# Kernel optimization log

Measured on AMD Instinct MI355X. Metric: run time of the kernel, lower is better.

## Reference

```python
import jax, jax.numpy as jnp
import numpy as np

B, S, D, H = 1, 2048, 1024, 16
DH = D // H  # 64
HID = 4 * D
EPS = 1e-5
NEG = -1.0e9


def setup_inputs() -> dict:
    key = jax.random.key(0)
    ks = jax.random.split(key, 12)
    s = 0.02
    return {
        "y": jax.random.normal(ks[0], (B, S, D), jnp.float32),
        "encoder_output": jax.random.normal(ks[1], (B, S, D), jnp.float32),
        # per-head shared projection (query_fc used for q,k,v — faithful to source bug)
        "Wq_self": jax.random.normal(ks[2], (H, D, DH), jnp.float32) * s,
        "bq_self": jax.random.normal(ks[3], (H, DH), jnp.float32) * s,
        "Wq_cross": jax.random.normal(ks[4], (H, D, DH), jnp.float32) * s,
        "bq_cross": jax.random.normal(ks[5], (H, DH), jnp.float32) * s,
        "g1": jnp.ones((D,), jnp.float32), "beta1": jnp.zeros((D,), jnp.float32),
        "g2": jnp.ones((D,), jnp.float32), "beta2": jnp.zeros((D,), jnp.float32),
        "g3": jnp.ones((D,), jnp.float32), "beta3": jnp.zeros((D,), jnp.float32),
        "w1": jax.random.normal(ks[6], (D, HID), jnp.float32) * s,
        "b1": jax.random.normal(ks[7], (HID,), jnp.float32) * s,
        "w2": jax.random.normal(ks[8], (HID, D), jnp.float32) * s,
        "b2": jax.random.normal(ks[9], (D,), jnp.float32) * s,
    }


def _layernorm(x, g, b):
    mu = jnp.mean(x, axis=-1, keepdims=True)
    var = jnp.mean((x - mu) ** 2, axis=-1, keepdims=True)
    return (x - mu) * jax.lax.rsqrt(var + EPS) * g + b


def _mha(x_q, x_kv, W, bias, causal):
    # source bug: q, k, v all use query_fc projection
    q = jnp.einsum('bsd,hde->bhse', x_q, W) + bias[None, :, None, :]
    k = jnp.einsum('bsd,hde->bhse', x_kv, W) + bias[None, :, None, :]
    v = jnp.einsum('bsd,hde->bhse', x_kv, W) + bias[None, :, None, :]
    scores = jnp.einsum('bhse,bhte->bhst', q, k) / jnp.sqrt(jnp.float32(DH))
    if causal:
        sq, sk = scores.shape[-2], scores.shape[-1]
        mask = jnp.triu(jnp.ones((sq, sk), bool), k=1)
        scores = jnp.where(mask, NEG, scores)
    p = jax.nn.softmax(scores, axis=-1)
    out = jnp.einsum('bhst,bhte->bhse', p, v)  # [B,H,S,DH]
    b, h, s, e = out.shape
    return out.transpose(0, 2, 1, 3).reshape(b, s, h * e)


def reference(y, encoder_output, Wq_self, bq_self, Wq_cross, bq_cross,
              g1, beta1, g2, beta2, g3, beta3, w1, b1, w2, b2):
    sa = _mha(y, y, Wq_self, bq_self, causal=True)
    y1 = _layernorm(y + sa, g1, beta1)
    ca = _mha(y1, encoder_output, Wq_cross, bq_cross, causal=False)
    y2 = _layernorm(y1 + ca, g2, beta2)
    ff = jnp.maximum(y2 @ w1 + b1, 0.0) @ w2 + b2
    return _layernorm(y2 + ff, g3, beta3)
```

## Files before the change

### kernel.cpp

```cpp
#include <hip/hip_runtime.h>
#include <hip/hip_bf16.h>


#define S_LEN 2048
#define DMODEL 1024
#define NHEAD 16
#define DHEAD 64
#define HIDDEN 4096

using bf16 = __hip_bfloat16;
typedef __attribute__((ext_vector_type(8))) short bf16x8;
typedef __attribute__((ext_vector_type(4))) float floatx4;

__device__ __forceinline__ void async_ld16(const void* g, void* l) {
  __builtin_amdgcn_global_load_lds(
      (const __attribute__((address_space(1))) unsigned int*)g,
      (__attribute__((address_space(3))) unsigned int*)l, 16, 0, 0);
}

__device__ __forceinline__ unsigned short f2bf_bits(float f) {
  __hip_bfloat16 b = __float2bfloat16(f);
  return *(unsigned short*)&b;
}

template <bool HEADB>
__global__ __launch_bounds__(256) void transp_bf16_kernel(
    const float* __restrict__ src0, bf16* __restrict__ dst0,
    const float* __restrict__ src1, bf16* __restrict__ dst1, int K, int N) {
  const float* src = blockIdx.z ? src1 : src0;
  bf16* dst = blockIdx.z ? dst1 : dst0;
  __shared__ float tile[32][33];
  const int tx = threadIdx.x & 31, ty = threadIdx.x >> 5;
  const int k0 = blockIdx.y * 32, n0 = blockIdx.x * 32;
#pragma unroll
  for (int i = 0; i < 4; ++i) {
    const int k = k0 + ty + i * 8;
    const int n = n0 + tx;
    size_t idx;
    if (HEADB)
      idx = (size_t)(n >> 6) * ((size_t)K * 64) + (size_t)k * 64 + (n & 63);
    else
      idx = (size_t)k * N + n;
    tile[ty + i * 8][tx] = src[idx];
  }
  __syncthreads();
#pragma unroll
  for (int i = 0; i < 4; ++i) {
    const int n = n0 + ty + i * 8;
    const int k = k0 + tx;
    dst[(size_t)n * K + k] = __float2bfloat16(tile[tx][ty + i * 8]);
  }
}

__global__ __launch_bounds__(256) void conv_bf16_kernel(
    const float* __restrict__ src0, bf16* __restrict__ dst0,
    const float* __restrict__ src1, bf16* __restrict__ dst1, int n4) {
  const float* src = blockIdx.z ? src1 : src0;
  bf16* dst = blockIdx.z ? dst1 : dst0;
  const int i = blockIdx.x * 256 + threadIdx.x;
  if (i >= n4) return;
  float4 v = ((const float4*)src)[i];
  unsigned short r[4] = {f2bf_bits(v.x), f2bf_bits(v.y), f2bf_bits(v.z), f2bf_bits(v.w)};
  ((ushort2*)dst)[i * 2] = make_ushort2(r[0], r[1]);
  ((ushort2*)dst)[i * 2 + 1] = make_ushort2(r[2], r[3]);
}

template <int BM, int BN, bool RELU, bool DUALT, typename CT>
__global__ __launch_bounds__(256) void mfma_gemm_kernel(
    const bf16* __restrict__ A0, const bf16* __restrict__ Bt0,
    const float* __restrict__ bias0, CT* __restrict__ C0,
    bf16* __restrict__ Ct0,
    const bf16* __restrict__ A1, const bf16* __restrict__ Bt1,
    const float* __restrict__ bias1, CT* __restrict__ C1,
    bf16* __restrict__ Ct1,
    int M, int N, int Kstride, int Klen) {
  const bf16* A = blockIdx.z ? A1 : A0;
  const bf16* Bt = blockIdx.z ? Bt1 : Bt0;
  const float* bias = blockIdx.z ? bias1 : bias0;
  CT* C = blockIdx.z ? C1 : C0;
  bf16* Ct = blockIdx.z ? Ct1 : Ct0;

  constexpr int MF = BM / 32;
  constexpr int NF = BN / 32;
  __shared__ __align__(16) bf16 As[2][BM * 64];
  __shared__ __align__(16) bf16 Bs[2][BN * 64];

  const int tid = threadIdx.x;
  const int wave = tid >> 6;
  const int lane = tid & 63;
  const int m0 = blockIdx.y * BM;
  const int n0 = blockIdx.x * BN;
  const int wr = wave >> 1, wc = wave & 1;

  const int srow = tid >> 3;
  const int schunk = (tid & 7) ^ (srow & 7);
  const bf16* agp = A + (size_t)(m0 + srow) * Kstride + schunk * 8;
  const bf16* bgp = Bt + (size_t)(n0 + srow) * Kstride + schunk * 8;

  floatx4 acc[MF][NF];
#pragma unroll
  for (int i = 0; i < MF; ++i)
#pragma unroll
    for (int j = 0; j < NF; ++j) acc[i][j] = floatx4{0.f, 0.f, 0.f, 0.f};

  const int mrow = lane & 15;
  const int p0 = (((lane >> 4) ^ (mrow & 7)) << 4);
  const int p1 = p0 ^ 64;

  auto stage = [&](int buf, int kt) {
    char* al = (char*)As + buf * (BM * 128) + wave * 1024;
    char* bl = (char*)Bs + buf * (BN * 128) + wave * 1024;
#pragma unroll
    for (int i = 0; i < BM / 32; ++i)
      async_ld16(agp + (size_t)(32 * i) * Kstride + kt, al + i * 4096);
#pragma unroll
    for (int i = 0; i < BN / 32; ++i)
      async_ld16(bgp + (size_t)(32 * i) * Kstride + kt, bl + i * 4096);
  };

  stage(0, 0);
  __syncthreads();

  int cur = 0;
  for (int kt = 0; kt < Klen; kt += 64) {
    if (kt + 64 < Klen) stage(cur ^ 1, kt + 64);

    const char* abase = (const char*)As + cur * (BM * 128);
    const char* bbase = (const char*)Bs + cur * (BN * 128);
    bf16x8 af0[MF], af1[MF], bf0[NF], bf1[NF];
#pragma unroll
    for (int fi = 0; fi < MF; ++fi) {
      const char* ar = abase + (wr * (BM / 2) + fi * 16 + mrow) * 128;
      af0[fi] = *(const bf16x8*)(ar + p0);
      af1[fi] = *(const bf16x8*)(ar + p1);
    }
#pragma unroll
    for (int fj = 0; fj < NF; ++fj) {
      const char* br = bbase + (wc * (BN / 2) + fj * 16 + mrow) * 128;
      bf0[fj] = *(const bf16x8*)(br + p0);
      bf1[fj] = *(const bf16x8*)(br + p1);
    }
#pragma unroll
    for (int fi = 0; fi < MF; ++fi)
#pragma unroll
      for (int fj = 0; fj < NF; ++fj) {
        acc[fi][fj] = __builtin_amdgcn_mfma_f32_16x16x32_bf16(
            af0[fi], bf0[fj], acc[fi][fj], 0, 0, 0);
        acc[fi][fj] = __builtin_amdgcn_mfma_f32_16x16x32_bf16(
            af1[fi], bf1[fj], acc[fi][fj], 0, 0, 0);
      }

    __syncthreads();
    cur ^= 1;
  }

  const int erow = (lane >> 4) * 4;
  const int ecol = lane & 15;
#pragma unroll
  for (int fi = 0; fi < MF; ++fi) {
#pragma unroll
    for (int fj = 0; fj < NF; ++fj) {
      const int nn = n0 + wc * (BN / 2) + fj * 16 + ecol;
      const float bv = bias ? bias[nn] : 0.0f;
      const int mmb = m0 + wr * (BM / 2) + fi * 16 + erow;
      float v[4];
#pragma unroll
      for (int r = 0; r < 4; ++r) {
        v[r] = acc[fi][fj][r] + bv;
        if (RELU) v[r] = fmaxf(v[r], 0.0f);
        if constexpr (sizeof(CT) == 2)
          C[(size_t)(mmb + r) * N + nn] = (CT)__float2bfloat16(v[r]);
        else
          C[(size_t)(mmb + r) * N + nn] = (CT)v[r];
      }
      if (DUALT) {
        ushort4 pk;
        pk.x = f2bf_bits(v[0]);
        pk.y = f2bf_bits(v[1]);
        pk.z = f2bf_bits(v[2]);
        pk.w = f2bf_bits(v[3]);
        *(ushort4*)&Ct[(size_t)nn * M + mmb] = pk;
      }
    }
  }
}

__global__ __launch_bounds__(128) void mfma_attn_kernel(
    const bf16* __restrict__ Q, const bf16* __restrict__ K,
    const bf16* __restrict__ Vt,
    float* __restrict__ OA, float* __restrict__ OB,
    float* __restrict__ LA, float* __restrict__ LB, int causal) {
  __shared__ __align__(16) unsigned short Kt[2][64 * 64];
  __shared__ __align__(16) unsigned short Vs[2][64 * 64];
  __shared__ __align__(16) unsigned short Ps[2][2048];

  const int tid = threadIdx.x;
  const int w = tid >> 6, lane = tid & 63;
  const int g = lane >> 4, c = lane & 15;
  const int h = blockIdx.y;
  const int qb = causal ? ((int)gridDim.x - 1 - (int)blockIdx.x)
                        : (int)blockIdx.x;
  const int q0 = qb * 64;
  const int z = blockIdx.z;
  const int qw = q0 + w * 32;
  float* Oz = z ? OB : OA;
  float* Lz = z ? LB : LA;

  bf16x8 qf0[2], qf1[2];
#pragma unroll
  for (int qs = 0; qs < 2; ++qs) {
    const bf16* qrow =
        Q + (size_t)(qw + qs * 16 + c) * DMODEL + h * DHEAD + g * 8;
    qf0[qs] = *(const bf16x8*)qrow;
    qf1[qs] = *(const bf16x8*)(qrow + 32);
  }

  const int srow = tid >> 3;
  const int schunk = (tid & 7) ^ (srow & 7);
  const bf16* kgp = K + (size_t)srow * DMODEL + h * DHEAD + schunk * 8;
  const bf16* vgp = Vt + (size_t)(h * DHEAD + srow) * S_LEN + schunk * 8;

  const int kpos0 = ((g ^ (c & 7)) << 4);
  const int kpos1 = kpos0 ^ 64;

  floatx4 of[4][2];
#pragma unroll
  for (int md = 0; md < 4; ++md)
#pragma unroll
    for (int qs = 0; qs < 2; ++qs) of[md][qs] = floatx4{0.f, 0.f, 0.f, 0.f};
  float lpart[2] = {0.f, 0.f};

  const int nkt = causal ? (q0 / 64 + 1) : (S_LEN / 64);

  auto stage = [&](int buf, int kt) {
    const int t0 = kt * 64;
    char* klds = (char*)Kt + buf * 8192 + w * 1024;
    char* vlds = (char*)Vs + buf * 8192 + w * 1024;
#pragma unroll
    for (int i = 0; i < 4; ++i) {
      async_ld16(kgp + (size_t)(t0 + 16 * i) * DMODEL, klds + i * 2048);
      async_ld16(vgp + (size_t)(16 * i) * S_LEN + t0, vlds + i * 2048);
    }
  };

  if (z < nkt) stage(0, z);
  __syncthreads();

  int cur = 0;
  for (int kt = z; kt < nkt; kt += 2) {
    const int t0 = kt * 64;
    if (kt + 2 < nkt) stage(cur ^ 1, kt + 2);

    const char* kbase = (const char*)Kt + cur * 8192;
    const char* vbase = (const char*)Vs + cur * 8192;

    const bool diag = causal && (t0 == q0);
#pragma unroll
    for (int jt = 0; jt < 4; ++jt) {
      const char* kr = kbase + (16 * jt + c) * 128;
      const bf16x8 kf0 = *(const bf16x8*)(kr + kpos0);
      const bf16x8 kf1 = *(const bf16x8*)(kr + kpos1);
#pragma unroll
      for (int qs = 0; qs < 2; ++qs) {
        floatx4 s = floatx4{0.f, 0.f, 0.f, 0.f};
        __builtin_amdgcn_s_setprio(1);
        s = __builtin_amdgcn_mfma_f32_16x16x32_bf16(kf0, qf0[qs], s, 0, 0, 0);
        s = __builtin_amdgcn_mfma_f32_16x16x32_bf16(kf1, qf1[qs], s, 0, 0, 0);
        __builtin_amdgcn_s_setprio(0);

        ushort4 pk;
        unsigned short* pp = (unsigned short*)&pk;
#pragma unroll
        for (int r = 0; r < 4; ++r) {
          float p = __expf(0.125f * s[r]);
          if (diag && (t0 + 16 * jt + 4 * g + r > qw + qs * 16 + c)) p = 0.0f;
          lpart[qs] += p;
          pp[r] = f2bf_bits(p);
        }
        const int qq = qs * 16 + c;
        const int pb = qq * 128 + ((8 * (4 * jt + g)) ^ ((qq & 7) << 4));
        *(ushort4*)((char*)Ps[w] + pb) = pk;
      }
    }

#pragma unroll
    for (int ks = 0; ks < 2; ++ks) {
      const int px = (64 * ks + 16 * g) ^ ((c & 7) << 4);
      const bf16x8 pf0 = *(const bf16x8*)((const char*)Ps[w] + c * 128 + px);
      const bf16x8 pf1 =
          *(const bf16x8*)((const char*)Ps[w] + (16 + c) * 128 + px);
      const int vpos = ks ? kpos1 : kpos0;
#pragma unroll
      for (int md = 0; md < 4; ++md) {
        const bf16x8 vf = *(const bf16x8*)(vbase + (md * 16 + c) * 128 + vpos);
        __builtin_amdgcn_s_setprio(1);
        of[md][0] = __builtin_amdgcn_mfma_f32_16x16x32_bf16(vf, pf0, of[md][0], 0, 0, 0);
        of[md][1] = __builtin_amdgcn_mfma_f32_16x16x32_bf16(vf, pf1, of[md][1], 0, 0, 0);
        __builtin_amdgcn_s_setprio(0);
      }
    }

    __syncthreads();
    cur ^= 1;
  }

#pragma unroll
  for (int qs = 0; qs < 2; ++qs) {
    lpart[qs] += __shfl_xor(lpart[qs], 16, 64);
    lpart[qs] += __shfl_xor(lpart[qs], 32, 64);
    if (g == 0) Lz[(size_t)h * S_LEN + qw + qs * 16 + c] = lpart[qs];
    float* orow = Oz + (size_t)(qw + qs * 16 + c) * DMODEL + h * DHEAD;
#pragma unroll
    for (int md = 0; md < 4; ++md) {
      float4 v;
      v.x = of[md][qs][0];
      v.y = of[md][qs][1];
      v.z = of[md][qs][2];
      v.w = of[md][qs][3];
      *(float4*)(orow + md * 16 + 4 * g) = v;
    }
  }
}

template <bool DUAL, bool MERGE, bool SUM2>
__global__ __launch_bounds__(256) void add_ln_kernel(
    const float* __restrict__ X, const float* __restrict__ R,
    const float* __restrict__ R2, const float* __restrict__ bvec,
    const float* __restrict__ La, const float* __restrict__ Lb,
    const float* __restrict__ g, const float* __restrict__ beta,
    float* __restrict__ out, bf16* __restrict__ out2) {
  const int row = blockIdx.x;
  const int tid = threadIdx.x;

  float v[4];
  float s1 = 0.0f, s2 = 0.0f;
#pragma unroll
  for (int i = 0; i < 4; ++i) {
    const int c = tid + i * 256;
    float x = X[(size_t)row * DMODEL + c];
    if (MERGE) {
      const int h = c >> 6;
      const float rl =
          1.0f / (La[(size_t)h * S_LEN + row] + Lb[(size_t)h * S_LEN + row]);
      x += (R[(size_t)row * DMODEL + c] + R2[(size_t)row * DMODEL + c]) * rl;
    } else if (SUM2) {
      x += R[(size_t)row * DMODEL + c] + R2[(size_t)row * DMODEL + c] + bvec[c];
    } else {
      x += R[(size_t)row * DMODEL + c];
    }
    v[i] = x;
    s1 += x;
    s2 += x * x;
  }
#pragma unroll
  for (int off = 32; off; off >>= 1) {
    s1 += __shfl_xor(s1, off, 64);
    s2 += __shfl_xor(s2, off, 64);
  }
  __shared__ float w1s[4], w2s[4];
  const int wid = tid >> 6, lane = tid & 63;
  if (lane == 0) { w1s[wid] = s1; w2s[wid] = s2; }
  __syncthreads();
  s1 = w1s[0] + w1s[1] + w1s[2] + w1s[3];
  s2 = w2s[0] + w2s[1] + w2s[2] + w2s[3];

  const float mu = s1 * (1.0f / DMODEL);
  const float var = s2 * (1.0f / DMODEL) - mu * mu;
  const float rstd = rsqrtf(var + 1e-5f);

#pragma unroll
  for (int i = 0; i < 4; ++i) {
    const int c = tid + i * 256;
    const float r = (v[i] - mu) * rstd * g[c] + beta[c];
    out[(size_t)row * DMODEL + c] = r;
    if (DUAL) out2[(size_t)row * DMODEL + c] = __float2bfloat16(r);
  }
}

extern "C" void kernel_launch(void* const* d_in, const int* in_sizes, int n_in,
                              void* d_out, int out_size, void* d_ws, size_t ws_size,
                              hipStream_t stream) {
  const float* y      = (const float*)d_in[0];
  const float* enc    = (const float*)d_in[1];
  const float* Wself  = (const float*)d_in[2];
  const float* bself  = (const float*)d_in[3];
  const float* Wcross = (const float*)d_in[4];
  const float* bcross = (const float*)d_in[5];
  const float* g1     = (const float*)d_in[6];
  const float* be1    = (const float*)d_in[7];
  const float* g2     = (const float*)d_in[8];
  const float* be2    = (const float*)d_in[9];
  const float* g3     = (const float*)d_in[10];
  const float* be3    = (const float*)d_in[11];
  const float* w1     = (const float*)d_in[12];
  const float* b1     = (const float*)d_in[13];
  const float* w2     = (const float*)d_in[14];
  const float* b2     = (const float*)d_in[15];
  float* out = (float*)d_out;

  char* ws = (char*)d_ws;
  const size_t MB = 1024 * 1024;
  bf16*  ybf   = (bf16*)(ws + 0 * MB);
  bf16*  encbf = (bf16*)(ws + 4 * MB);
  float* PA    = (float*)(ws + 0 * MB);
  float* PB    = (float*)(ws + 8 * MB);
  float* Y1    = (float*)(ws + 16 * MB);
  float* Y2    = (float*)(ws + 24 * MB);
  bf16*  Q12b  = (bf16*)(ws + 32 * MB);
  bf16*  Q1t   = (bf16*)(ws + 36 * MB);
  bf16*  K2b   = (bf16*)(ws + 40 * MB);
  bf16*  K2t   = (bf16*)(ws + 44 * MB);
  bf16*  w1t   = (bf16*)(ws + 48 * MB);
  bf16*  w2t   = (bf16*)(ws + 56 * MB);
  bf16*  Wst   = (bf16*)(ws + 64 * MB);
  bf16*  Wct   = (bf16*)(ws + 66 * MB);
  bf16*  Y1bf  = (bf16*)(ws + 68 * MB);
  bf16*  Y2bf  = (bf16*)(ws + 72 * MB);
  float* La    = (float*)(ws + 76 * MB);
  float* Lb    = (float*)(ws + 76 * MB + 512 * 1024);
  bf16*  FFH   = (bf16*)(ws + 0 * MB);
  float* FFa   = (float*)(ws + 32 * MB);
  float* FFb   = (float*)(ws + 40 * MB);

  const dim3 blk(256);
  const dim3 blkA(128);
  const dim3 gT_w(DMODEL / 32, DMODEL / 32, 2);
  const dim3 gT_w1(HIDDEN / 32, DMODEL / 32);
  const dim3 gT_w2(DMODEL / 32, HIDDEN / 32);
  const dim3 gConv(S_LEN * DMODEL / 4 / 256, 1, 2);
  const dim3 gProj2(DMODEL / 64, S_LEN / 64, 2);
  const dim3 gProj(DMODEL / 64, S_LEN / 64);
  const dim3 gFf1(HIDDEN / 128, S_LEN / 64);
  const dim3 gFf2(DMODEL / 64, S_LEN / 64, 2);
  const dim3 gAttn(S_LEN / 64, NHEAD, 2);
  const dim3 gLn(S_LEN);

  transp_bf16_kernel<true><<<gT_w, blk, 0, stream>>>(
      Wself, Wst, Wcross, Wct, DMODEL, DMODEL);
  transp_bf16_kernel<false><<<gT_w1, blk, 0, stream>>>(
      w1, w1t, nullptr, nullptr, DMODEL, HIDDEN);
  transp_bf16_kernel<false><<<gT_w2, blk, 0, stream>>>(
      w2, w2t, nullptr, nullptr, HIDDEN, DMODEL);
  conv_bf16_kernel<<<gConv, blk, 0, stream>>>(
      y, ybf, enc, encbf, S_LEN * DMODEL / 4);

  mfma_gemm_kernel<64, 64, false, true, bf16><<<gProj2, blk, 0, stream>>>(
      ybf, Wst, bself, Q12b, Q1t,
      encbf, Wct, bcross, K2b, K2t, S_LEN, DMODEL, DMODEL, DMODEL);
  mfma_attn_kernel<<<gAttn, blkA, 0, stream>>>(
      Q12b, Q12b, Q1t, PA, PB, La, Lb, 1);
  add_ln_kernel<true, true, false><<<gLn, blk, 0, stream>>>(
      y, PA, PB, nullptr, La, Lb, g1, be1, Y1, Y1bf);
  mfma_gemm_kernel<64, 64, false, false, bf16><<<gProj, blk, 0, stream>>>(
      Y1bf, Wct, bcross, Q12b, nullptr,
      nullptr, nullptr, nullptr, nullptr, nullptr, S_LEN, DMODEL, DMODEL, DMODEL);
  mfma_attn_kernel<<<gAttn, blkA, 0, stream>>>(
      Q12b, K2b, K2t, PA, PB, La, Lb, 0);
  add_ln_kernel<true, true, false><<<gLn, blk, 0, stream>>>(
      Y1, PA, PB, nullptr, La, Lb, g2, be2, Y2, Y2bf);
  mfma_gemm_kernel<64, 128, true, false, bf16><<<gFf1, blk, 0, stream>>>(
      Y2bf, w1t, b1, FFH, nullptr,
      nullptr, nullptr, nullptr, nullptr, nullptr, S_LEN, HIDDEN, DMODEL, DMODEL);
  mfma_gemm_kernel<64, 64, false, false, float><<<gFf2, blk, 0, stream>>>(
      FFH, w2t, nullptr, FFa, nullptr,
      FFH + HIDDEN / 2, w2t + HIDDEN / 2, nullptr, FFb, nullptr,
      S_LEN, DMODEL, HIDDEN, HIDDEN / 2);
  add_ln_kernel<false, false, true><<<gLn, blk, 0, stream>>>(
      Y2, FFa, FFb, b2, nullptr, nullptr, g3, be3, out, nullptr);
}
```

Measured before the change: 313.8 us.

## Restructure attention into 4 waves with 32-key tiles and smaller GEMM tiles

The attention kernel now uses 256 threads, with each of the 4 waves owning 16 query rows. It streams 32-key K/V tiles with smaller LDS buffers and skips waves that lie entirely above the causal diagonal. The aim is more concurrent waves and less wasted causal work, at the cost of more loop iterations and more barriers per key. Separately, the GEMM now issues the next-tile prefetch after reading the current fragments from LDS. The Q-projection and FF1 GEMMs also switch to smaller tiles, giving more blocks at the cost of less reuse per block.

```diff
diff --git a/kernel.cpp b/kernel.cpp
--- a/kernel.cpp
+++ b/kernel.cpp
@@ -80,7 +80,7 @@
   CT* C = blockIdx.z ? C1 : C0;
   bf16* Ct = blockIdx.z ? Ct1 : Ct0;
 
-  constexpr int MF = BM / 32;
+  constexpr int MF = (BM + 31) / 32;
   constexpr int NF = BN / 32;
   __shared__ __align__(16) bf16 As[2][BM * 64];
   __shared__ __align__(16) bf16 Bs[2][BN * 64];
@@ -123,8 +123,6 @@
 
   int cur = 0;
   for (int kt = 0; kt < Klen; kt += 64) {
-    if (kt + 64 < Klen) stage(cur ^ 1, kt + 64);
-
     const char* abase = (const char*)As + cur * (BM * 128);
     const char* bbase = (const char*)Bs + cur * (BN * 128);
     bf16x8 af0[MF], af1[MF], bf0[NF], bf1[NF];
@@ -140,6 +138,9 @@
       bf0[fj] = *(const bf16x8*)(br + p0);
       bf1[fj] = *(const bf16x8*)(br + p1);
     }
+
+    if (kt + 64 < Klen) stage(cur ^ 1, kt + 64);
+
 #pragma unroll
     for (int fi = 0; fi < MF; ++fi)
 #pragma unroll
@@ -185,14 +186,14 @@
   }
 }
 
-__global__ __launch_bounds__(128) void mfma_attn_kernel(
+__global__ __launch_bounds__(256) void mfma_attn_kernel(
     const bf16* __restrict__ Q, const bf16* __restrict__ K,
     const bf16* __restrict__ Vt,
     float* __restrict__ OA, float* __restrict__ OB,
     float* __restrict__ LA, float* __restrict__ LB, int causal) {
-  __shared__ __align__(16) unsigned short Kt[2][64 * 64];
-  __shared__ __align__(16) unsigned short Vs[2][64 * 64];
-  __shared__ __align__(16) unsigned short Ps[2][2048];
+  __shared__ __align__(16) unsigned short Kt[2][32 * 64];
+  __shared__ __align__(16) unsigned short Vs[2][64 * 32];
+  __shared__ __align__(16) unsigned short Ps[4][512];
 
   const int tid = threadIdx.x;
   const int w = tid >> 6, lane = tid & 63;
@@ -202,70 +203,73 @@
                         : (int)blockIdx.x;
   const int q0 = qb * 64;
   const int z = blockIdx.z;
-  const int qw = q0 + w * 32;
+  const int qw = q0 + w * 16;
   float* Oz = z ? OB : OA;
   float* Lz = z ? LB : LA;
 
-  bf16x8 qf0[2], qf1[2];
-#pragma unroll
-  for (int qs = 0; qs < 2; ++qs) {
-    const bf16* qrow =
-        Q + (size_t)(qw + qs * 16 + c) * DMODEL + h * DHEAD + g * 8;
-    qf0[qs] = *(const bf16x8*)qrow;
-    qf1[qs] = *(const bf16x8*)(qrow + 32);
-  }
-
-  const int srow = tid >> 3;
-  const int schunk = (tid & 7) ^ (srow & 7);
-  const bf16* kgp = K + (size_t)srow * DMODEL + h * DHEAD + schunk * 8;
-  const bf16* vgp = Vt + (size_t)(h * DHEAD + srow) * S_LEN + schunk * 8;
+  const bf16* qrow = Q + (size_t)(qw + c) * DMODEL + h * DHEAD + g * 8;
+  const bf16x8 qfa = *(const bf16x8*)qrow;
+  const bf16x8 qfb = *(const bf16x8*)(qrow + 32);
+
+  const int srk = tid >> 3;
+  const int sck = (tid & 7) ^ (srk & 7);
+  const bf16* kgp = K + (size_t)srk * DMODEL + h * DHEAD + sck * 8;
+  const int srv = tid >> 2;
+  const int scv = (tid & 3) ^ ((srv >> 1) & 3);
+  const bf16* vgp = Vt + (size_t)(h * DHEAD + srv) * S_LEN + scv * 8;
 
   const int kpos0 = ((g ^ (c & 7)) << 4);
   const int kpos1 = kpos0 ^ 64;
-
-  floatx4 of[4][2];
-#pragma unroll
-  for (int md = 0; md < 4; ++md)
-#pragma unroll
-    for (int qs = 0; qs < 2; ++qs) of[md][qs] = floatx4{0.f, 0.f, 0.f, 0.f};
-  float lpart[2] = {0.f, 0.f};
-
-  const int nkt = causal ? (q0 / 64 + 1) : (S_LEN / 64);
+  const int vpos = ((g ^ ((c >> 1) & 3)) << 4);
+  char* pswave = (char*)Ps + w * 1024;
+
+  floatx4 of[4];
+#pragma unroll
+  for (int md = 0; md < 4; ++md) of[md] = floatx4{0.f, 0.f, 0.f, 0.f};
+  float lpart = 0.f;
+
+  const int nkt = causal ? (q0 / 32 + 2) : (S_LEN / 32);
 
   auto stage = [&](int buf, int kt) {
-    const int t0 = kt * 64;
-    char* klds = (char*)Kt + buf * 8192 + w * 1024;
-    char* vlds = (char*)Vs + buf * 8192 + w * 1024;
-#pragma unroll
-    for (int i = 0; i < 4; ++i) {
-      async_ld16(kgp + (size_t)(t0 + 16 * i) * DMODEL, klds + i * 2048);
-      async_ld16(vgp + (size_t)(16 * i) * S_LEN + t0, vlds + i * 2048);
-    }
+    const int t0 = kt * 32;
+    async_ld16(kgp + (size_t)t0 * DMODEL, (char*)Kt + buf * 4096 + w * 1024);
+    async_ld16(vgp + t0, (char*)Vs + buf * 4096 + w * 1024);
   };
 
-  if (z < nkt) stage(0, z);
+  stage(0, z);
   __syncthreads();
 
   int cur = 0;
   for (int kt = z; kt < nkt; kt += 2) {
-    const int t0 = kt * 64;
+    const int t0 = kt * 32;
+    const bool act = !(causal && t0 >= qw + 16);
+
+    bf16x8 kf00, kf01, kf10, kf11, vf0, vf1, vf2, vf3;
+    if (act) {
+      const char* kbase = (const char*)Kt + cur * 4096;
+      const char* vbase = (const char*)Vs + cur * 4096;
+      const char* kr0 = kbase + c * 128;
+      const char* kr1 = kbase + (16 + c) * 128;
+      kf00 = *(const bf16x8*)(kr0 + kpos0);
+      kf01 = *(const bf16x8*)(kr0 + kpos1);
+      kf10 = *(const bf16x8*)(kr1 + kpos0);
+      kf11 = *(const bf16x8*)(kr1 + kpos1);
+      vf0 = *(const bf16x8*)(vbase + (c)*64 + vpos);
+      vf1 = *(const bf16x8*)(vbase + (16 + c) * 64 + vpos);
+      vf2 = *(const bf16x8*)(vbase + (32 + c) * 64 + vpos);
+      vf3 = *(const bf16x8*)(vbase + (48 + c) * 64 + vpos);
+    }
+
     if (kt + 2 < nkt) stage(cur ^ 1, kt + 2);
 
-    const char* kbase = (const char*)Kt + cur * 8192;
-    const char* vbase = (const char*)Vs + cur * 8192;
-
-    const bool diag = causal && (t0 == q0);
-#pragma unroll
-    for (int jt = 0; jt < 4; ++jt) {
-      const char* kr = kbase + (16 * jt + c) * 128;
-      const bf16x8 kf0 = *(const bf16x8*)(kr + kpos0);
-      const bf16x8 kf1 = *(const bf16x8*)(kr + kpos1);
-#pragma unroll
-      for (int qs = 0; qs < 2; ++qs) {
+    if (act) {
+      const bool diag = causal && (t0 + 32 > qw);
+#pragma unroll
+      for (int jt = 0; jt < 2; ++jt) {
         floatx4 s = floatx4{0.f, 0.f, 0.f, 0.f};
         __builtin_amdgcn_s_setprio(1);
-        s = __builtin_amdgcn_mfma_f32_16x16x32_bf16(kf0, qf0[qs], s, 0, 0, 0);
-        s = __builtin_amdgcn_mfma_f32_16x16x32_bf16(kf1, qf1[qs], s, 0, 0, 0);
+        s = __builtin_amdgcn_mfma_f32_16x16x32_bf16(jt ? kf10 : kf00, qfa, s, 0, 0, 0);
+        s = __builtin_amdgcn_mfma_f32_16x16x32_bf16(jt ? kf11 : kf01, qfb, s, 0, 0, 0);
         __builtin_amdgcn_s_setprio(0);
 
         ushort4 pk;
@@ -273,52 +277,41 @@
 #pragma unroll
         for (int r = 0; r < 4; ++r) {
           float p = __expf(0.125f * s[r]);
-          if (diag && (t0 + 16 * jt + 4 * g + r > qw + qs * 16 + c)) p = 0.0f;
-          lpart[qs] += p;
+          if (diag && (t0 + 16 * jt + 4 * g + r > qw + c)) p = 0.0f;
+          lpart += p;
           pp[r] = f2bf_bits(p);
         }
-        const int qq = qs * 16 + c;
-        const int pb = qq * 128 + ((8 * (4 * jt + g)) ^ ((qq & 7) << 4));
-        *(ushort4*)((char*)Ps[w] + pb) = pk;
+        const int pb =
+            c * 64 + ((((2 * jt + (g >> 1)) ^ ((c >> 1) & 3)) << 4) |
+                      ((g & 1) << 3));
+        *(ushort4*)(pswave + pb) = pk;
       }
-    }
-
-#pragma unroll
-    for (int ks = 0; ks < 2; ++ks) {
-      const int px = (64 * ks + 16 * g) ^ ((c & 7) << 4);
-      const bf16x8 pf0 = *(const bf16x8*)((const char*)Ps[w] + c * 128 + px);
-      const bf16x8 pf1 =
-          *(const bf16x8*)((const char*)Ps[w] + (16 + c) * 128 + px);
-      const int vpos = ks ? kpos1 : kpos0;
-#pragma unroll
-      for (int md = 0; md < 4; ++md) {
-        const bf16x8 vf = *(const bf16x8*)(vbase + (md * 16 + c) * 128 + vpos);
-        __builtin_amdgcn_s_setprio(1);
-        of[md][0] = __builtin_amdgcn_mfma_f32_16x16x32_bf16(vf, pf0, of[md][0], 0, 0, 0);
-        of[md][1] = __builtin_amdgcn_mfma_f32_16x16x32_bf16(vf, pf1, of[md][1], 0, 0, 0);
-        __builtin_amdgcn_s_setprio(0);
-      }
+
+      const bf16x8 pf = *(const bf16x8*)(pswave + c * 64 + vpos);
+      __builtin_amdgcn_s_setprio(1);
+      of[0] = __builtin_amdgcn_mfma_f32_16x16x32_bf16(vf0, pf, of[0], 0, 0, 0);
+      of[1] = __builtin_amdgcn_mfma_f32_16x16x32_bf16(vf1, pf, of[1], 0, 0, 0);
+      of[2] = __builtin_amdgcn_mfma_f32_16x16x32_bf16(vf2, pf, of[2], 0, 0, 0);
+      of[3] = __builtin_amdgcn_mfma_f32_16x16x32_bf16(vf3, pf, of[3], 0, 0, 0);
+      __builtin_amdgcn_s_setprio(0);
     }
 
     __syncthreads();
     cur ^= 1;
   }
 
-#pragma unroll
-  for (int qs = 0; qs < 2; ++qs) {
-    lpart[qs] += __shfl_xor(lpart[qs], 16, 64);
-    lpart[qs] += __shfl_xor(lpart[qs], 32, 64);
-    if (g == 0) Lz[(size_t)h * S_LEN + qw + qs * 16 + c] = lpart[qs];
-    float* orow = Oz + (size_t)(qw + qs * 16 + c) * DMODEL + h * DHEAD;
-#pragma unroll
-    for (int md = 0; md < 4; ++md) {
-      float4 v;
-      v.x = of[md][qs][0];
-      v.y = of[md][qs][1];
-      v.z = of[md][qs][2];
-      v.w = of[md][qs][3];
-      *(float4*)(orow + md * 16 + 4 * g) = v;
-    }
+  lpart += __shfl_xor(lpart, 16, 64);
+  lpart += __shfl_xor(lpart, 32, 64);
+  if (g == 0) Lz[(size_t)h * S_LEN + qw + c] = lpart;
+  float* orow = Oz + (size_t)(qw + c) * DMODEL + h * DHEAD;
+#pragma unroll
+  for (int md = 0; md < 4; ++md) {
+    float4 v;
+    v.x = of[md][0];
+    v.y = of[md][1];
+    v.z = of[md][2];
+    v.w = of[md][3];
+    *(float4*)(orow + md * 16 + 4 * g) = v;
   }
 }
 
@@ -423,14 +416,13 @@
   float* FFb   = (float*)(ws + 40 * MB);
 
   const dim3 blk(256);
-  const dim3 blkA(128);
   const dim3 gT_w(DMODEL / 32, DMODEL / 32, 2);
   const dim3 gT_w1(HIDDEN / 32, DMODEL / 32);
   const dim3 gT_w2(DMODEL / 32, HIDDEN / 32);
   const dim3 gConv(S_LEN * DMODEL / 4 / 256, 1, 2);
   const dim3 gProj2(DMODEL / 64, S_LEN / 64, 2);
-  const dim3 gProj(DMODEL / 64, S_LEN / 64);
-  const dim3 gFf1(HIDDEN / 128, S_LEN / 64);
+  const dim3 gProj(DMODEL / 64, S_LEN / 32);
+  const dim3 gFf1(HIDDEN / 64, S_LEN / 64);
   const dim3 gFf2(DMODEL / 64, S_LEN / 64, 2);
   const dim3 gAttn(S_LEN / 64, NHEAD, 2);
   const dim3 gLn(S_LEN);
@@ -447,18 +439,18 @@
   mfma_gemm_kernel<64, 64, false, true, bf16><<<gProj2, blk, 0, stream>>>(
       ybf, Wst, bself, Q12b, Q1t,
       encbf, Wct, bcross, K2b, K2t, S_LEN, DMODEL, DMODEL, DMODEL);
-  mfma_attn_kernel<<<gAttn, blkA, 0, stream>>>(
+  mfma_attn_kernel<<<gAttn, blk, 0, stream>>>(
       Q12b, Q12b, Q1t, PA, PB, La, Lb, 1);
   add_ln_kernel<true, true, false><<<gLn, blk, 0, stream>>>(
       y, PA, PB, nullptr, La, Lb, g1, be1, Y1, Y1bf);
-  mfma_gemm_kernel<64, 64, false, false, bf16><<<gProj, blk, 0, stream>>>(
+  mfma_gemm_kernel<32, 64, false, false, bf16><<<gProj, blk, 0, stream>>>(
       Y1bf, Wct, bcross, Q12b, nullptr,
       nullptr, nullptr, nullptr, nullptr, nullptr, S_LEN, DMODEL, DMODEL, DMODEL);
-  mfma_attn_kernel<<<gAttn, blkA, 0, stream>>>(
+  mfma_attn_kernel<<<gAttn, blk, 0, stream>>>(
       Q12b, K2b, K2t, PA, PB, La, Lb, 0);
   add_ln_kernel<true, true, false><<<gLn, blk, 0, stream>>>(
       Y1, PA, PB, nullptr, La, Lb, g2, be2, Y2, Y2bf);
-  mfma_gemm_kernel<64, 128, true, false, bf16><<<gFf1, blk, 0, stream>>>(
+  mfma_gemm_kernel<64, 64, true, false, bf16><<<gFf1, blk, 0, stream>>>(
       Y2bf, w1t, b1, FFH, nullptr,
       nullptr, nullptr, nullptr, nullptr, nullptr, S_LEN, HIDDEN, DMODEL, DMODEL);
   mfma_gemm_kernel<64, 64, false, false, float><<<gFf2, blk, 0, stream>>>(
```

Result: faster. 306.6 us (-2.3%).
